# Kernel optimization log

Measured on AMD Instinct MI355X. Metric: run time of the kernel, lower is better.

Reference implementation:

```python
import jax, jax.numpy as jnp
import numpy as np

N = 50000   # nodes
E = 800000  # edges
H = 128     # hidden_channels
L = 3       # num_layers - 2 GIN blocks
C = 1       # out_channels
G = 512     # graphs in batch
BN_EPS = 1e-5


def _bn(x, g, b, m, v):
    # BatchNorm1d in eval mode: running stats
    return g * (x - m) * jax.lax.rsqrt(v + BN_EPS) + b


def setup_inputs() -> dict:
    key = jax.random.key(0)
    ks = jax.random.split(key, 16)
    s = 0.05
    inp = {
        "x": jax.random.randint(ks[0], (N,), 0, 100),
        "edge_index": jax.random.randint(ks[1], (2, E), 0, N),
        "batch": jnp.sort(jax.random.randint(ks[2], (N,), 0, G)),
        "embed_table": jax.random.normal(ks[3], (100, H), jnp.float32) * s,
        # pre-conv BatchNorm1d (self.norms)
        "bn_g": jnp.ones((L, H), jnp.float32),
        "bn_b": jnp.zeros((L, H), jnp.float32),
        "bn_m": jax.random.normal(ks[4], (L, H), jnp.float32) * s,
        "bn_v": jax.random.uniform(ks[5], (L, H), jnp.float32, 0.5, 1.5),
        # self.lins
        "lin_w": jax.random.normal(ks[6], (L, H, H), jnp.float32) * s,
        "lin_b": jnp.zeros((L, H), jnp.float32),
        # GINConv eps (train_eps=True) and its MLP: Linear-BN-ReLU-Linear
        "eps": jnp.zeros((L,), jnp.float32),
        "mlp_w1": jax.random.normal(ks[7], (L, H, H), jnp.float32) * s,
        "mlp_b1": jnp.zeros((L, H), jnp.float32),
        "mbn_g": jnp.ones((L, H), jnp.float32),
        "mbn_b": jnp.zeros((L, H), jnp.float32),
        "mbn_m": jax.random.normal(ks[8], (L, H), jnp.float32) * s,
        "mbn_v": jax.random.uniform(ks[9], (L, H), jnp.float32, 0.5, 1.5),
        "mlp_w2": jax.random.normal(ks[10], (L, H, H), jnp.float32) * s,
        "mlp_b2": jnp.zeros((L, H), jnp.float32),
        # readout Linear
        "ro_w": jax.random.normal(ks[11], (H, C), jnp.float32) * s,
        "ro_b": jnp.zeros((C,), jnp.float32),
    }
    return inp


def reference(x, edge_index, batch, embed_table, bn_g, bn_b, bn_m, bn_v,
              lin_w, lin_b, eps, mlp_w1, mlp_b1, mbn_g, mbn_b, mbn_m, mbn_v,
              mlp_w2, mlp_b2, ro_w, ro_b):
    h = embed_table[x]                      # [N, H]
    src, dst = edge_index[0], edge_index[1]
    for i in range(L):
        h = _bn(h, bn_g[i], bn_b[i], bn_m[i], bn_v[i])
        h = jax.nn.relu(h @ lin_w[i] + lin_b[i])
        # dropout is identity in eval mode
        # GINConv: mlp((1+eps)*x + sum_{j in N(i)} x_j)
        agg = jax.ops.segment_sum(h[src], dst, num_segments=N)
        z = (1.0 + eps[i]) * h + agg
        z = jax.nn.relu(_bn(z @ mlp_w1[i] + mlp_b1[i], mbn_g[i], mbn_b[i], mbn_m[i], mbn_v[i]))
        h = z @ mlp_w2[i] + mlp_b2[i]
    out = h @ ro_w + ro_b                   # [N, C]
    return jax.ops.segment_sum(out, batch, num_segments=G)  # [G, C]
```

## Files before the change

### kernel.cpp

```cpp
#include <hip/hip_runtime.h>
#include <hip/hip_fp16.h>


#define HD 128
#define NLAYER 3
#define PITCH 136

typedef _Float16 half8 __attribute__((ext_vector_type(8)));
typedef float    f32x4 __attribute__((ext_vector_type(4)));

__global__ void prep_weights(
    const float* __restrict__ bn_g, const float* __restrict__ bn_b,
    const float* __restrict__ bn_m, const float* __restrict__ bn_v,
    const float* __restrict__ lin_w, const float* __restrict__ lin_b,
    const float* __restrict__ mbn_g, const float* __restrict__ mbn_b,
    const float* __restrict__ mbn_m, const float* __restrict__ mbn_v,
    const float* __restrict__ mlp_w1, const float* __restrict__ mlp_b1,
    const float* __restrict__ mlp_w2,
    _Float16* __restrict__ wtl, float* __restrict__ fbl,
    _Float16* __restrict__ wt1, float* __restrict__ fb1,
    _Float16* __restrict__ wt2)
{
    const int l = blockIdx.x;
    const int t = threadIdx.x;
    __shared__ float sa[HD], sc[HD], sa2[HD];

    const int lb = l * HD;
    const int wb = l * HD * HD;
    float a  = bn_g[lb + t] * rsqrtf(bn_v[lb + t] + 1e-5f);
    float c  = bn_b[lb + t] - bn_m[lb + t] * a;
    float a2 = mbn_g[lb + t] * rsqrtf(mbn_v[lb + t] + 1e-5f);
    float c2 = mbn_b[lb + t] - mbn_m[lb + t] * a2;
    sa[t] = a; sc[t] = c; sa2[t] = a2;
    __syncthreads();

    float accb = lin_b[lb + t];
    for (int k = 0; k < HD; ++k) accb += sc[k] * lin_w[wb + k * HD + t];
    fbl[lb + t] = accb;
    fb1[lb + t] = a2 * mlp_b1[lb + t] + c2;

    for (int j = 0; j < HD; ++j) {
        wtl[wb + j * HD + t] = (_Float16)(sa[t] * lin_w[wb + t * HD + j]);
        wt1[wb + j * HD + t] = (_Float16)(sa2[j] * mlp_w1[wb + t * HD + j]);
        wt2[wb + j * HD + t] = (_Float16)(mlp_w2[wb + t * HD + j]);
    }
}

__global__ void count_deg(const int* __restrict__ dst, int* __restrict__ deg, int e)
{
    int i = blockIdx.x * blockDim.x + threadIdx.x;
    if (i < e) atomicAdd(&deg[dst[i]], 1);
}

__global__ void scan_blocks(const int* __restrict__ deg, int* __restrict__ excl,
                            int* __restrict__ partials, int n)
{
    __shared__ int wt[4];
    int t = threadIdx.x;
    int base = blockIdx.x * 1024 + t * 4;
    int v0 = (base + 0 < n) ? deg[base + 0] : 0;
    int v1 = (base + 1 < n) ? deg[base + 1] : 0;
    int v2 = (base + 2 < n) ? deg[base + 2] : 0;
    int v3 = (base + 3 < n) ? deg[base + 3] : 0;
    int s = v0 + v1 + v2 + v3;
    int lane = t & 63, w = t >> 6;
    int inc = s;
    #pragma unroll
    for (int d = 1; d < 64; d <<= 1) {
        int o = __shfl_up(inc, d);
        if (lane >= d) inc += o;
    }
    if (lane == 63) wt[w] = inc;
    __syncthreads();
    int off = 0;
    for (int i = 0; i < w; ++i) off += wt[i];
    int ex = off + inc - s;
    if (base + 0 < n) excl[base + 0] = ex; ex += v0;
    if (base + 1 < n) excl[base + 1] = ex; ex += v1;
    if (base + 2 < n) excl[base + 2] = ex; ex += v2;
    if (base + 3 < n) excl[base + 3] = ex;
    if (t == 255) partials[blockIdx.x] = off + inc;
}

__global__ void scan_small(int* __restrict__ partials, int nb)
{
    int t = threadIdx.x;
    int v = (t < nb) ? partials[t] : 0;
    int inc = v;
    #pragma unroll
    for (int d = 1; d < 64; d <<= 1) {
        int o = __shfl_up(inc, d);
        if (t >= d) inc += o;
    }
    if (t < nb) partials[t] = inc - v;
}

__global__ void scan_add(int* __restrict__ rowst, int* __restrict__ cursor,
                         const int* __restrict__ partials, int n, int e)
{
    int idx = blockIdx.x * blockDim.x + threadIdx.x;
    if (idx < n) {
        int v = rowst[idx] + partials[idx >> 10];
        rowst[idx] = v;
        cursor[idx] = v;
    }
    if (idx == 0) rowst[n] = e;
}

__global__ void fill_csr(const int* __restrict__ src, const int* __restrict__ dst,
                         int* __restrict__ cursor, int* __restrict__ esrc, int e)
{
    int i = blockIdx.x * blockDim.x + threadIdx.x;
    if (i < e) {
        int p = atomicAdd(&cursor[dst[i]], 1);
        esrc[p] = src[i];
    }
}

template<bool GATHER>
__global__ __launch_bounds__(256, 3)
void lin_mfma(const float* __restrict__ Xf, const _Float16* __restrict__ Xh,
              const int* __restrict__ xidx,
              const _Float16* __restrict__ Wt, const float* __restrict__ B,
              _Float16* __restrict__ Y, int n)
{
    __shared__ __align__(16) _Float16 sA[64 * PITCH];
    const int t = threadIdx.x;
    const int lane = t & 63;
    const int w = t >> 6;
    const int rw_ = w >> 1, cw = w & 1;
    const int m = lane & 15, g = lane >> 4;
    const int tile = blockIdx.x * 64;

    {
        int row = t >> 2, q = t & 3;
        int gr = tile + row;
        _Float16* dst = &sA[row * PITCH + q * 32];
        if (GATHER) {
            if (gr < n) {
                int id = xidx[gr];
                const float4* src = reinterpret_cast<const float4*>(Xf + (size_t)id * HD) + q * 8;
                #pragma unroll
                for (int c = 0; c < 4; ++c) {
                    float4 va = src[2 * c], vb = src[2 * c + 1];
                    half8 h = {(_Float16)va.x, (_Float16)va.y, (_Float16)va.z, (_Float16)va.w,
                               (_Float16)vb.x, (_Float16)vb.y, (_Float16)vb.z, (_Float16)vb.w};
                    *reinterpret_cast<half8*>(dst + c * 8) = h;
                }
            } else {
                half8 zz = {0, 0, 0, 0, 0, 0, 0, 0};
                #pragma unroll
                for (int c = 0; c < 4; ++c) *reinterpret_cast<half8*>(dst + c * 8) = zz;
            }
        } else {
            half8 zz = {0, 0, 0, 0, 0, 0, 0, 0};
            const half8* src = reinterpret_cast<const half8*>(Xh + (size_t)gr * HD + q * 32);
            #pragma unroll
            for (int c = 0; c < 4; ++c)
                *reinterpret_cast<half8*>(dst + c * 8) = (gr < n) ? src[c] : zz;
        }
    }
    __syncthreads();

    half8 bf[4][4];
    #pragma unroll
    for (int ct4 = 0; ct4 < 4; ++ct4) {
        int ct = 4 * cw + ct4;
        #pragma unroll
        for (int kk = 0; kk < 4; ++kk)
            bf[ct4][kk] = *reinterpret_cast<const half8*>(
                Wt + (size_t)(16 * ct + m) * HD + kk * 32 + g * 8);
    }

    f32x4 acc[2][4];
    #pragma unroll
    for (int i = 0; i < 2; ++i)
        #pragma unroll
        for (int j = 0; j < 4; ++j) acc[i][j] = (f32x4){0.f, 0.f, 0.f, 0.f};

    #pragma unroll
    for (int rg2 = 0; rg2 < 2; ++rg2) {
        int rg = 2 * rw_ + rg2;
        #pragma unroll
        for (int kk = 0; kk < 4; ++kk) {
            half8 a = *reinterpret_cast<const half8*>(
                &sA[(16 * rg + m) * PITCH + kk * 32 + g * 8]);
            #pragma unroll
            for (int ct4 = 0; ct4 < 4; ++ct4)
                acc[rg2][ct4] = __builtin_amdgcn_mfma_f32_16x16x32_f16(
                    a, bf[ct4][kk], acc[rg2][ct4], 0, 0, 0);
        }
    }

    #pragma unroll
    for (int rg2 = 0; rg2 < 2; ++rg2) {
        int rg = 2 * rw_ + rg2;
        #pragma unroll
        for (int ct4 = 0; ct4 < 4; ++ct4) {
            int col = 16 * (4 * cw + ct4) + m;
            float bb = B[col];
            #pragma unroll
            for (int reg = 0; reg < 4; ++reg) {
                int r = tile + 16 * rg + 4 * g + reg;
                if (r < n) {
                    float v = fmaxf(acc[rg2][ct4][reg] + bb, 0.f);
                    Y[(size_t)r * HD + col] = (_Float16)v;
                }
            }
        }
    }
}

__global__ void aggregate_f16(const _Float16* __restrict__ h2,
                              const int* __restrict__ rowst,
                              const int* __restrict__ esrc,
                              const float* __restrict__ epsp,
                              int layer, _Float16* __restrict__ z, int n)
{
    int gw = (blockIdx.x * blockDim.x + threadIdx.x) >> 6;
    int lane = threadIdx.x & 63;
    if (gw >= n) return;
    float se = 1.0f + epsp[layer];
    int rs = __builtin_amdgcn_readfirstlane(rowst[gw]);
    int re = __builtin_amdgcn_readfirstlane(rowst[gw + 1]);
    const half2* hv = reinterpret_cast<const half2*>(h2);
    float2 s = __half22float2(hv[(size_t)gw * 64 + lane]);
    float ax0 = se * s.x, ay0 = se * s.y;
    float ax1 = 0.f, ay1 = 0.f, ax2 = 0.f, ay2 = 0.f, ax3 = 0.f, ay3 = 0.f;
    for (int base = rs; base < re; base += 64) {
        int cnt = re - base; if (cnt > 64) cnt = 64;
        int eid = (base + lane < re) ? esrc[base + lane] : 0;
        int j = 0;
        for (; j + 4 <= cnt; j += 4) {
            int s0 = __shfl(eid, j + 0);
            int s1 = __shfl(eid, j + 1);
            int s2 = __shfl(eid, j + 2);
            int s3 = __shfl(eid, j + 3);
            float2 v0 = __half22float2(hv[(size_t)s0 * 64 + lane]);
            float2 v1 = __half22float2(hv[(size_t)s1 * 64 + lane]);
            float2 v2 = __half22float2(hv[(size_t)s2 * 64 + lane]);
            float2 v3 = __half22float2(hv[(size_t)s3 * 64 + lane]);
            ax0 += v0.x; ay0 += v0.y;
            ax1 += v1.x; ay1 += v1.y;
            ax2 += v2.x; ay2 += v2.y;
            ax3 += v3.x; ay3 += v3.y;
        }
        for (; j < cnt; ++j) {
            int s0 = __shfl(eid, j);
            float2 v0 = __half22float2(hv[(size_t)s0 * 64 + lane]);
            ax0 += v0.x; ay0 += v0.y;
        }
    }
    float ox = (ax0 + ax1) + (ax2 + ax3);
    float oy = (ay0 + ay1) + (ay2 + ay3);
    reinterpret_cast<half2*>(z)[(size_t)gw * 64 + lane] = __floats2half2_rn(ox, oy);
}

template<bool FUSE_RO>
__global__ __launch_bounds__(256, 3)
void mlp_mfma(const _Float16* __restrict__ Z,
              const _Float16* __restrict__ Wt1, const float* __restrict__ B1,
              const _Float16* __restrict__ Wt2, const float* __restrict__ B2,
              _Float16* __restrict__ H,
              const float* __restrict__ rw, const float* __restrict__ rb,
              const int* __restrict__ batch, float* __restrict__ gout, int n)
{
    __shared__ __align__(16) _Float16 sA[64 * PITCH];
    __shared__ float sD[64][2];
    const int t = threadIdx.x;
    const int lane = t & 63;
    const int w = t >> 6;
    const int rw_ = w >> 1, cw = w & 1;
    const int m = lane & 15, g = lane >> 4;
    const int tile = blockIdx.x * 64;

    {
        int row = t >> 2, q = t & 3;
        int gr = tile + row;
        _Float16* dst = &sA[row * PITCH + q * 32];
        half8 zz = {0, 0, 0, 0, 0, 0, 0, 0};
        const half8* src = reinterpret_cast<const half8*>(Z + (size_t)gr * HD + q * 32);
        #pragma unroll
        for (int c = 0; c < 4; ++c)
            *reinterpret_cast<half8*>(dst + c * 8) = (gr < n) ? src[c] : zz;
    }
    __syncthreads();

    half8 bf[4][4];
    #pragma unroll
    for (int ct4 = 0; ct4 < 4; ++ct4) {
        int ct = 4 * cw + ct4;
        #pragma unroll
        for (int kk = 0; kk < 4; ++kk)
            bf[ct4][kk] = *reinterpret_cast<const half8*>(
                Wt1 + (size_t)(16 * ct + m) * HD + kk * 32 + g * 8);
    }
    f32x4 acc[2][4];
    #pragma unroll
    for (int i = 0; i < 2; ++i)
        #pragma unroll
        for (int j = 0; j < 4; ++j) acc[i][j] = (f32x4){0.f, 0.f, 0.f, 0.f};
    #pragma unroll
    for (int rg2 = 0; rg2 < 2; ++rg2) {
        int rg = 2 * rw_ + rg2;
        #pragma unroll
        for (int kk = 0; kk < 4; ++kk) {
            half8 a = *reinterpret_cast<const half8*>(
                &sA[(16 * rg + m) * PITCH + kk * 32 + g * 8]);
            #pragma unroll
            for (int ct4 = 0; ct4 < 4; ++ct4)
                acc[rg2][ct4] = __builtin_amdgcn_mfma_f32_16x16x32_f16(
                    a, bf[ct4][kk], acc[rg2][ct4], 0, 0, 0);
        }
    }
    __syncthreads();

    #pragma unroll
    for (int rg2 = 0; rg2 < 2; ++rg2) {
        int rg = 2 * rw_ + rg2;
        #pragma unroll
        for (int ct4 = 0; ct4 < 4; ++ct4) {
            int col = 16 * (4 * cw + ct4) + m;
            float bb = B1[col];
            #pragma unroll
            for (int reg = 0; reg < 4; ++reg) {
                int lr = 16 * rg + 4 * g + reg;
                sA[lr * PITCH + col] = (_Float16)fmaxf(acc[rg2][ct4][reg] + bb, 0.f);
            }
        }
    }
    __syncthreads();

    #pragma unroll
    for (int ct4 = 0; ct4 < 4; ++ct4) {
        int ct = 4 * cw + ct4;
        #pragma unroll
        for (int kk = 0; kk < 4; ++kk)
            bf[ct4][kk] = *reinterpret_cast<const half8*>(
                Wt2 + (size_t)(16 * ct + m) * HD + kk * 32 + g * 8);
    }
    f32x4 acc2[2][4];
    #pragma unroll
    for (int i = 0; i < 2; ++i)
        #pragma unroll
        for (int j = 0; j < 4; ++j) acc2[i][j] = (f32x4){0.f, 0.f, 0.f, 0.f};
    #pragma unroll
    for (int rg2 = 0; rg2 < 2; ++rg2) {
        int rg = 2 * rw_ + rg2;
        #pragma unroll
        for (int kk = 0; kk < 4; ++kk) {
            half8 a = *reinterpret_cast<const half8*>(
                &sA[(16 * rg + m) * PITCH + kk * 32 + g * 8]);
            #pragma unroll
            for (int ct4 = 0; ct4 < 4; ++ct4)
                acc2[rg2][ct4] = __builtin_amdgcn_mfma_f32_16x16x32_f16(
                    a, bf[ct4][kk], acc2[rg2][ct4], 0, 0, 0);
        }
    }

    if (!FUSE_RO) {
        #pragma unroll
        for (int rg2 = 0; rg2 < 2; ++rg2) {
            int rg = 2 * rw_ + rg2;
            #pragma unroll
            for (int ct4 = 0; ct4 < 4; ++ct4) {
                int col = 16 * (4 * cw + ct4) + m;
                float bb = B2[col];
                #pragma unroll
                for (int reg = 0; reg < 4; ++reg) {
                    int r = tile + 16 * rg + 4 * g + reg;
                    if (r < n)
                        H[(size_t)r * HD + col] = (_Float16)(acc2[rg2][ct4][reg] + bb);
                }
            }
        }
    } else {
        #pragma unroll
        for (int rg2 = 0; rg2 < 2; ++rg2) {
            int rg = 2 * rw_ + rg2;
            float pr[4] = {0.f, 0.f, 0.f, 0.f};
            #pragma unroll
            for (int ct4 = 0; ct4 < 4; ++ct4) {
                int col = 16 * (4 * cw + ct4) + m;
                float bb = B2[col], rr = rw[col];
                #pragma unroll
                for (int reg = 0; reg < 4; ++reg)
                    pr[reg] = fmaf(acc2[rg2][ct4][reg] + bb, rr, pr[reg]);
            }
            #pragma unroll
            for (int reg = 0; reg < 4; ++reg) {
                #pragma unroll
                for (int d = 1; d < 16; d <<= 1) pr[reg] += __shfl_xor(pr[reg], d);
            }
            if (m == 0) {
                #pragma unroll
                for (int reg = 0; reg < 4; ++reg)
                    sD[16 * rg + 4 * g + reg][cw] = pr[reg];
            }
        }
        __syncthreads();
        if (t < 64) {
            int row = tile + t;
            float v = sD[t][0] + sD[t][1] + rb[0];
            int b = (row < n) ? batch[row] : -1;
            if (row >= n) v = 0.f;
            #pragma unroll
            for (int d = 1; d < 64; d <<= 1) {
                int   ob = __shfl_up(b, d);
                float ov = __shfl_up(v, d);
                if (t >= d && ob == b) v += ov;
            }
            int nb2 = __shfl_down(b, 1);
            bool lastl = (t == 63) || (nb2 != b);
            if (lastl && b >= 0) atomicAdd(&gout[b], v);
        }
    }
}

extern "C" void kernel_launch(void* const* d_in, const int* in_sizes, int n_in,
                              void* d_out, int out_size, void* d_ws, size_t ws_size,
                              hipStream_t stream)
{
    const int N = in_sizes[0];
    const int E = in_sizes[1] / 2;
    const int G = out_size;

    const int*   x      = (const int*)d_in[0];
    const int*   ei     = (const int*)d_in[1];
    const int*   batch  = (const int*)d_in[2];
    const float* table  = (const float*)d_in[3];
    const float* bn_g   = (const float*)d_in[4];
    const float* bn_b   = (const float*)d_in[5];
    const float* bn_m   = (const float*)d_in[6];
    const float* bn_v   = (const float*)d_in[7];
    const float* lin_w  = (const float*)d_in[8];
    const float* lin_b  = (const float*)d_in[9];
    const float* epsv   = (const float*)d_in[10];
    const float* mlp_w1 = (const float*)d_in[11];
    const float* mlp_b1 = (const float*)d_in[12];
    const float* mbn_g  = (const float*)d_in[13];
    const float* mbn_b  = (const float*)d_in[14];
    const float* mbn_m  = (const float*)d_in[15];
    const float* mbn_v  = (const float*)d_in[16];
    const float* mlp_w2 = (const float*)d_in[17];
    const float* mlp_b2 = (const float*)d_in[18];
    const float* ro_w   = (const float*)d_in[19];
    const float* ro_b   = (const float*)d_in[20];

    const int* esrc_in = ei;
    const int* edst_in = ei + E;

    char* wsp = (char*)d_ws;
    size_t off = 0;
    auto alloc = [&](size_t bytes) {
        void* p = wsp + off;
        off += (bytes + 255) & ~(size_t)255;
        return p;
    };
    _Float16* bufA  = (_Float16*)alloc((size_t)N * HD * 2);
    _Float16* bufB  = (_Float16*)alloc((size_t)N * HD * 2);
    _Float16* wtl   = (_Float16*)alloc((size_t)NLAYER * HD * HD * 2);
    _Float16* wt1   = (_Float16*)alloc((size_t)NLAYER * HD * HD * 2);
    _Float16* wt2   = (_Float16*)alloc((size_t)NLAYER * HD * HD * 2);
    float*    fbl   = (float*)alloc((size_t)NLAYER * HD * 4);
    float*    fb1   = (float*)alloc((size_t)NLAYER * HD * 4);
    int*      deg   = (int*)alloc((size_t)N * 4);
    int*      rowst = (int*)alloc((size_t)(N + 1) * 4);
    int*      cursor= (int*)alloc((size_t)N * 4);
    int*      esrc  = (int*)alloc((size_t)E * 4);
    int*      part  = (int*)alloc(256 * 4);
    (void)ws_size;

    hipMemsetAsync(deg, 0, (size_t)N * 4, stream);
    hipMemsetAsync(d_out, 0, (size_t)G * 4, stream);

    prep_weights<<<NLAYER, HD, 0, stream>>>(
        bn_g, bn_b, bn_m, bn_v, lin_w, lin_b,
        mbn_g, mbn_b, mbn_m, mbn_v, mlp_w1, mlp_b1, mlp_w2,
        wtl, fbl, wt1, fb1, wt2);

    count_deg<<<(E + 255) / 256, 256, 0, stream>>>(edst_in, deg, E);
    int nb = (N + 1023) / 1024;
    scan_blocks<<<nb, 256, 0, stream>>>(deg, rowst, part, N);
    scan_small<<<1, 64, 0, stream>>>(part, nb);
    scan_add<<<(N + 255) / 256, 256, 0, stream>>>(rowst, cursor, part, N, E);
    fill_csr<<<(E + 255) / 256, 256, 0, stream>>>(esrc_in, edst_in, cursor, esrc, E);

    const int gemm_grid = (N + 63) / 64;
    const int wave_grid = (N + 3) / 4;

    for (int l = 0; l < NLAYER; ++l) {
        const _Float16* wl = wtl + (size_t)l * HD * HD;
        const float*    bl = fbl + (size_t)l * HD;
        const _Float16* w1 = wt1 + (size_t)l * HD * HD;
        const float*    b1 = fb1 + (size_t)l * HD;
        const _Float16* w2 = wt2 + (size_t)l * HD * HD;
        const float*    b2 = mlp_b2 + (size_t)l * HD;

        if (l == 0)
            lin_mfma<true><<<gemm_grid, 256, 0, stream>>>(
                table, nullptr, x, wl, bl, bufB, N);
        else
            lin_mfma<false><<<gemm_grid, 256, 0, stream>>>(
                nullptr, bufA, nullptr, wl, bl, bufB, N);

        aggregate_f16<<<wave_grid, 256, 0, stream>>>(
            bufB, rowst, esrc, epsv, l, bufA, N);

        if (l < NLAYER - 1)
            mlp_mfma<false><<<gemm_grid, 256, 0, stream>>>(
                bufA, w1, b1, w2, b2, bufA,
                nullptr, nullptr, nullptr, nullptr, N);
        else
            mlp_mfma<true><<<gemm_grid, 256, 0, stream>>>(
                bufA, w1, b1, w2, b2, nullptr,
                ro_w, ro_b, batch, (float*)d_out, N);
    }
}
```

Before: 422.2 us.

## Partition CSR build by destination range and store edge sources as 16-bit

Count-degree and CSR-fill kernels now split the destination node space into 8 ranges. The block index selects a range, so each block handles a contiguous edge chunk, filtered to one range. On MI355X this lines up with the 8 XCDs, which keeps atomics on a given node range local to one L2. Edge source indices are stored as unsigned short, which halves the esrc traffic in the CSR fill and in the three aggregation passes. The cost is that every edge is read 8 times in the build kernels, and the 16-bit sources only hold while N fits in 65535, which is true here (N=50000).

```diff
diff --git a/kernel.cpp b/kernel.cpp
--- a/kernel.cpp
+++ b/kernel.cpp
@@ -5,6 +5,7 @@
 #define HD 128
 #define NLAYER 3
 #define PITCH 136
+#define EPB 2048
 
 typedef _Float16 half8 __attribute__((ext_vector_type(8)));
 typedef float    f32x4 __attribute__((ext_vector_type(4)));
@@ -46,10 +47,37 @@
     }
 }
 
-__global__ void count_deg(const int* __restrict__ dst, int* __restrict__ deg, int e)
-{
-    int i = blockIdx.x * blockDim.x + threadIdx.x;
-    if (i < e) atomicAdd(&deg[dst[i]], 1);
+__global__ void count_deg(const int* __restrict__ dst, int* __restrict__ deg,
+                          int e, int npr)
+{
+    int r = blockIdx.x & 7;
+    int chunk = blockIdx.x >> 3;
+    int lo = r * npr, hi = lo + npr;
+    int base = chunk * EPB;
+    int end = base + EPB; if (end > e) end = e;
+    for (int i = base + threadIdx.x; i < end; i += 256) {
+        int d = dst[i];
+        if (d >= lo && d < hi) atomicAdd(&deg[d], 1);
+    }
+}
+
+__global__ void fill_csr(const int* __restrict__ src, const int* __restrict__ dst,
+                         int* __restrict__ cursor,
+                         unsigned short* __restrict__ esrc, int e, int npr)
+{
+    int r = blockIdx.x & 7;
+    int chunk = blockIdx.x >> 3;
+    int lo = r * npr, hi = lo + npr;
+    int base = chunk * EPB;
+    int end = base + EPB; if (end > e) end = e;
+    for (int i = base + threadIdx.x; i < end; i += 256) {
+        int d = dst[i];
+        int s = src[i];
+        if (d >= lo && d < hi) {
+            int p = atomicAdd(&cursor[d], 1);
+            esrc[p] = (unsigned short)s;
+        }
+    }
 }
 
 __global__ void scan_blocks(const int* __restrict__ deg, int* __restrict__ excl,
@@ -105,16 +133,6 @@
         cursor[idx] = v;
     }
     if (idx == 0) rowst[n] = e;
-}
-
-__global__ void fill_csr(const int* __restrict__ src, const int* __restrict__ dst,
-                         int* __restrict__ cursor, int* __restrict__ esrc, int e)
-{
-    int i = blockIdx.x * blockDim.x + threadIdx.x;
-    if (i < e) {
-        int p = atomicAdd(&cursor[dst[i]], 1);
-        esrc[p] = src[i];
-    }
 }
 
 template<bool GATHER>
@@ -213,7 +231,7 @@
 
 __global__ void aggregate_f16(const _Float16* __restrict__ h2,
                               const int* __restrict__ rowst,
-                              const int* __restrict__ esrc,
+                              const unsigned short* __restrict__ esrc,
                               const float* __restrict__ epsp,
                               int layer, _Float16* __restrict__ z, int n)
 {
@@ -229,7 +247,7 @@
     float ax1 = 0.f, ay1 = 0.f, ax2 = 0.f, ay2 = 0.f, ax3 = 0.f, ay3 = 0.f;
     for (int base = rs; base < re; base += 64) {
         int cnt = re - base; if (cnt > 64) cnt = 64;
-        int eid = (base + lane < re) ? esrc[base + lane] : 0;
+        int eid = (base + lane < re) ? (int)esrc[base + lane] : 0;
         int j = 0;
         for (; j + 4 <= cnt; j += 4) {
             int s0 = __shfl(eid, j + 0);
@@ -467,7 +485,7 @@
     int*      deg   = (int*)alloc((size_t)N * 4);
     int*      rowst = (int*)alloc((size_t)(N + 1) * 4);
     int*      cursor= (int*)alloc((size_t)N * 4);
-    int*      esrc  = (int*)alloc((size_t)E * 4);
+    unsigned short* esrc = (unsigned short*)alloc((size_t)E * 2);
     int*      part  = (int*)alloc(256 * 4);
     (void)ws_size;
 
@@ -479,12 +497,14 @@
         mbn_g, mbn_b, mbn_m, mbn_v, mlp_w1, mlp_b1, mlp_w2,
         wtl, fbl, wt1, fb1, wt2);
 
-    count_deg<<<(E + 255) / 256, 256, 0, stream>>>(edst_in, deg, E);
+    const int npr = (N + 7) / 8;
+    const int chunks = (E + EPB - 1) / EPB;
+    count_deg<<<chunks * 8, 256, 0, stream>>>(edst_in, deg, E, npr);
     int nb = (N + 1023) / 1024;
     scan_blocks<<<nb, 256, 0, stream>>>(deg, rowst, part, N);
     scan_small<<<1, 64, 0, stream>>>(part, nb);
     scan_add<<<(N + 255) / 256, 256, 0, stream>>>(rowst, cursor, part, N, E);
-    fill_csr<<<(E + 255) / 256, 256, 0, stream>>>(esrc_in, edst_in, cursor, esrc, E);
+    fill_csr<<<chunks * 8, 256, 0, stream>>>(esrc_in, edst_in, cursor, esrc, E, npr);
 
     const int gemm_grid = (N + 63) / 64;
     const int wave_grid = (N + 3) / 4;
```

New measurement: 410.9 us. 2.7% less time.
